# Kernel tuning notes

Hardware: AMD Instinct MI355X
Metric: run time of the kernel (lower is better)

The kernel has to match this reference:

```python
import jax, jax.numpy as jnp
import numpy as np

N_NODES = 100000
N_EDGES = 1600000
IN_DIM = 128
HID = 32
HEADS = 4
OUT_DIM = 64
NEG_SLOPE = 0.2


def gat_conv(src, dst, x, W, al, ar, b, activation):
    # x: [N, F_in], W: [F_in, H*D], al/ar: [H, D], b: [H*D]
    N = x.shape[0]
    H, D = al.shape
    h = (x @ W).reshape(N, H, D)                       # [N, H, D]
    el = jnp.einsum('nhd,hd->nh', h, al)               # [N, H]
    er = jnp.einsum('nhd,hd->nh', h, ar)               # [N, H]
    e = el[src] + er[dst]                              # [E, H]
    e = jnp.where(e > 0, e, NEG_SLOPE * e)             # leaky_relu(0.2)
    # segment softmax over destination nodes
    m = jax.ops.segment_max(e, dst, num_segments=N)    # [N, H]
    m = jnp.where(jnp.isfinite(m), m, 0.0)
    ee = jnp.exp(e - m[dst])                           # [E, H]
    denom = jax.ops.segment_sum(ee, dst, num_segments=N)  # [N, H]
    alpha = ee / denom[dst]                            # [E, H]
    msg = alpha[:, :, None] * h[src]                   # [E, H, D]
    out = jax.ops.segment_sum(msg, dst, num_segments=N)   # [N, H, D]
    out = out + b.reshape(1, H, D)
    if activation is not None:
        out = activation(out)
    return out


def setup_inputs() -> dict:
    key = jax.random.key(0)
    ks = jax.random.split(key, 16)
    hw = HID * HEADS  # 128
    ow = OUT_DIM * HEADS  # 256
    s = lambda fan: 1.0 / np.sqrt(fan)
    return {
        'nfeat': jax.random.normal(ks[0], (N_NODES, IN_DIM), jnp.float32),
        'src': jax.random.randint(ks[1], (N_EDGES,), 0, N_NODES),
        'dst': jax.random.randint(ks[2], (N_EDGES,), 0, N_NODES),
        'W0': jax.random.normal(ks[3], (IN_DIM, hw), jnp.float32) * s(IN_DIM),
        'al0': jax.random.normal(ks[4], (HEADS, HID), jnp.float32) * s(HID),
        'ar0': jax.random.normal(ks[5], (HEADS, HID), jnp.float32) * s(HID),
        'b0': jnp.zeros((hw,), jnp.float32),
        'W1': jax.random.normal(ks[6], (hw, hw), jnp.float32) * s(hw),
        'al1': jax.random.normal(ks[7], (HEADS, HID), jnp.float32) * s(HID),
        'ar1': jax.random.normal(ks[8], (HEADS, HID), jnp.float32) * s(HID),
        'b1': jnp.zeros((hw,), jnp.float32),
        'W2': jax.random.normal(ks[9], (hw, ow), jnp.float32) * s(hw),
        'al2': jax.random.normal(ks[10], (HEADS, OUT_DIM), jnp.float32) * s(OUT_DIM),
        'ar2': jax.random.normal(ks[11], (HEADS, OUT_DIM), jnp.float32) * s(OUT_DIM),
        'b2': jnp.zeros((ow,), jnp.float32),
    }


def reference(nfeat, src, dst, W0, al0, ar0, b0, W1, al1, ar1, b1, W2, al2, ar2, b2):
    h = nfeat
    # hidden layers: elu activation, flatten heads
    h = gat_conv(src, dst, h, W0, al0, ar0, b0, jax.nn.elu).reshape(N_NODES, -1)
    h = gat_conv(src, dst, h, W1, al1, ar1, b1, jax.nn.elu).reshape(N_NODES, -1)
    # output layer: no activation, mean over heads
    out = gat_conv(src, dst, h, W2, al2, ar2, b2, None).mean(axis=1)  # [N, OUT_DIM]
    return out
```

## Files before the change

kernel.cpp:

```cpp
#include <hip/hip_runtime.h>
#include <hip/hip_bf16.h>
#include <cstddef>
#include <cstdint>

#define N_NODES 100000
#define N_EDGES 1600000
#define NPASS 4

typedef __attribute__((ext_vector_type(8))) short bf16x8;
typedef __attribute__((ext_vector_type(4))) float f32x4;
typedef __attribute__((ext_vector_type(2))) _Float16 half2_t;
typedef __attribute__((ext_vector_type(4))) _Float16 half4_t;

__device__ inline unsigned short f2bf(float x) {
    unsigned int u = __float_as_uint(x);
    unsigned int r = (u + 0x7fffu + ((u >> 16) & 1u)) >> 16;
    return (unsigned short)r;
}
__device__ inline float bf2f(unsigned short b) {
    return __uint_as_float((unsigned int)b << 16);
}
__device__ inline unsigned short f2h_bits(float x) {
    _Float16 h = (_Float16)x;
    return __builtin_bit_cast(unsigned short, h);
}

__global__ void hist_kernel(const int* __restrict__ dst, int* __restrict__ deg) {
    int e = blockIdx.x * 256 + threadIdx.x;
    if (e < N_EDGES) atomicAdd(&deg[dst[e]], 1);
}

__global__ void scan_block_kernel(const int* __restrict__ deg, int* __restrict__ rowptr,
                                  int* __restrict__ bsum) {
    __shared__ int s[256];
    int t = threadIdx.x;
    int base = blockIdx.x * 1024 + t * 4;
    int v[4]; int sum = 0;
#pragma unroll
    for (int j = 0; j < 4; ++j) { v[j] = (base + j < N_NODES) ? deg[base + j] : 0; sum += v[j]; }
    s[t] = sum; __syncthreads();
    for (int off = 1; off < 256; off <<= 1) {
        int x = (t >= off) ? s[t - off] : 0;
        __syncthreads();
        s[t] += x;
        __syncthreads();
    }
    int excl = (t > 0) ? s[t - 1] : 0;
    if (t == 255) bsum[blockIdx.x] = s[255];
    int run = excl;
#pragma unroll
    for (int j = 0; j < 4; ++j) { if (base + j < N_NODES) rowptr[base + j] = run; run += v[j]; }
}

__global__ void scan_bsum_kernel(int* bsum, int nb) {
    __shared__ int s[128];
    int t = threadIdx.x;
    int v = (t < nb) ? bsum[t] : 0;
    s[t] = v; __syncthreads();
    for (int off = 1; off < 128; off <<= 1) {
        int x = (t >= off) ? s[t - off] : 0;
        __syncthreads();
        s[t] += x;
        __syncthreads();
    }
    if (t < nb) bsum[t] = (t > 0) ? s[t - 1] : 0;
}

__global__ void scan_add_kernel(int* __restrict__ rowptr, const int* __restrict__ bsum) {
    int i = blockIdx.x * 256 + threadIdx.x;
    if (i < N_NODES) rowptr[i] += bsum[i >> 10];
    if (i == 0) rowptr[N_NODES] = N_EDGES;
}

__global__ __launch_bounds__(256) void scatter_pass_kernel(
    const int* __restrict__ src, const int* __restrict__ dst,
    const int* __restrict__ rowptr, int* __restrict__ fill,
    int* __restrict__ csr_src, int lo, int hi) {
    int e = blockIdx.x * 256 + threadIdx.x;
    if (e >= N_EDGES) return;
    int d = dst[e];
    if (d >= lo && d < hi) {
        int pos = rowptr[d] + atomicAdd(&fill[d], 1);
        csr_src[pos] = src[e];
    }
}

__global__ __launch_bounds__(256) void convert_w_kernel(const float* __restrict__ W,
                                                        unsigned short* __restrict__ Wth,
                                                        unsigned short* __restrict__ Wtl,
                                                        int Ncols) {
    int t = blockIdx.x * 256 + threadIdx.x;
    if (t >= 128 * Ncols) return;
    int n = t >> 7, k = t & 127;
    float x = W[(size_t)k * Ncols + n];
    unsigned short h = f2bf(x);
    unsigned short l = f2bf(x - bf2f(h));
    Wth[t] = h;
    Wtl[t] = l;
}

template <int DHEAD, bool FP32IN>
__global__ __launch_bounds__(256) void mfma_gemm_kernel(
    const unsigned short* __restrict__ Xhi, const unsigned short* __restrict__ Xlo,
    const float* __restrict__ Xf,
    const unsigned short* __restrict__ Wth, const unsigned short* __restrict__ Wtl,
    float* __restrict__ el, float* __restrict__ er, _Float16* __restrict__ Hh,
    int M, int ldH, const float* __restrict__ alv, const float* __restrict__ arv) {
    __shared__ unsigned short AH[128 * 136];
    __shared__ unsigned short AL[128 * 136];
    const int tid = threadIdx.x;
    const int wave = tid >> 6, lane = tid & 63;
    const int r = lane & 15, kg = lane >> 4;
    const int row0 = blockIdx.x * 128;
    const int col0 = blockIdx.y * 128;

    if constexpr (FP32IN) {
#pragma unroll
        for (int i = 0; i < 16; ++i) {
            int idx = i * 256 + tid;
            int rr = idx >> 5;
            int u = idx & 31;
            int grow = row0 + rr;
            if (grow > M - 1) grow = M - 1;
            float4 v = *reinterpret_cast<const float4*>(Xf + (size_t)grow * 128 + u * 4);
            unsigned short h0 = f2bf(v.x), h1 = f2bf(v.y), h2 = f2bf(v.z), h3 = f2bf(v.w);
            unsigned short l0 = f2bf(v.x - bf2f(h0)), l1 = f2bf(v.y - bf2f(h1));
            unsigned short l2 = f2bf(v.z - bf2f(h2)), l3 = f2bf(v.w - bf2f(h3));
            unsigned int* hp = reinterpret_cast<unsigned int*>(&AH[rr * 136 + u * 4]);
            hp[0] = (unsigned int)h0 | ((unsigned int)h1 << 16);
            hp[1] = (unsigned int)h2 | ((unsigned int)h3 << 16);
            unsigned int* lp = reinterpret_cast<unsigned int*>(&AL[rr * 136 + u * 4]);
            lp[0] = (unsigned int)l0 | ((unsigned int)l1 << 16);
            lp[1] = (unsigned int)l2 | ((unsigned int)l3 << 16);
        }
    } else {
#pragma unroll
        for (int i = 0; i < 16; ++i) {
            int sa = i * 256 + tid;
            int a = sa >> 11;
            int s = sa & 2047;
            int rr = s >> 4;
            int u = s & 15;
            const unsigned short* srcp = (a ? Xlo : Xhi) + (size_t)(row0 + rr) * 128 + u * 8;
            unsigned short* dstp = (a ? AL : AH) + rr * 136 + u * 8;
            *reinterpret_cast<uint4*>(dstp) = *reinterpret_cast<const uint4*>(srcp);
        }
    }
    __syncthreads();

    f32x4 acc[2][8];
#pragma unroll
    for (int rt = 0; rt < 2; ++rt)
#pragma unroll
        for (int ct = 0; ct < 8; ++ct)
            acc[rt][ct] = (f32x4){0.f, 0.f, 0.f, 0.f};

#pragma unroll
    for (int ks = 0; ks < 4; ++ks) {
        bf16x8 bh[8], bl[8];
#pragma unroll
        for (int ct = 0; ct < 8; ++ct) {
            size_t off = (size_t)(col0 + ct * 16 + r) * 128 + ks * 32 + kg * 8;
            bh[ct] = *reinterpret_cast<const bf16x8*>(Wth + off);
            bl[ct] = *reinterpret_cast<const bf16x8*>(Wtl + off);
        }
#pragma unroll
        for (int rt = 0; rt < 2; ++rt) {
            int lrow = wave * 32 + rt * 16 + r;
            bf16x8 ah = *reinterpret_cast<const bf16x8*>(&AH[lrow * 136 + ks * 32 + kg * 8]);
            bf16x8 al8 = *reinterpret_cast<const bf16x8*>(&AL[lrow * 136 + ks * 32 + kg * 8]);
#pragma unroll
            for (int ct = 0; ct < 8; ++ct) {
                acc[rt][ct] = __builtin_amdgcn_mfma_f32_16x16x32_bf16(ah, bh[ct], acc[rt][ct], 0, 0, 0);
                acc[rt][ct] = __builtin_amdgcn_mfma_f32_16x16x32_bf16(al8, bh[ct], acc[rt][ct], 0, 0, 0);
                acc[rt][ct] = __builtin_amdgcn_mfma_f32_16x16x32_bf16(ah, bl[ct], acc[rt][ct], 0, 0, 0);
            }
        }
    }

    constexpr int CTH = DHEAD / 16;
    constexpr int HB = 8 / CTH;
    float als[8], ars[8];
#pragma unroll
    for (int ct = 0; ct < 8; ++ct) {
        als[ct] = alv[col0 + ct * 16 + r];
        ars[ct] = arv[col0 + ct * 16 + r];
    }
    f32x4 pel[2][HB], per_[2][HB];
#pragma unroll
    for (int rt = 0; rt < 2; ++rt)
#pragma unroll
        for (int hl = 0; hl < HB; ++hl) {
            pel[rt][hl] = (f32x4){0.f, 0.f, 0.f, 0.f};
            per_[rt][hl] = (f32x4){0.f, 0.f, 0.f, 0.f};
        }
#pragma unroll
    for (int rt = 0; rt < 2; ++rt)
#pragma unroll
        for (int ct = 0; ct < 8; ++ct) {
            pel[rt][ct / CTH] += acc[rt][ct] * als[ct];
            per_[rt][ct / CTH] += acc[rt][ct] * ars[ct];
        }
#pragma unroll
    for (int off = 1; off < 16; off <<= 1) {
#pragma unroll
        for (int rt = 0; rt < 2; ++rt)
#pragma unroll
            for (int hl = 0; hl < HB; ++hl)
#pragma unroll
                for (int j = 0; j < 4; ++j) {
                    pel[rt][hl][j] += __shfl_xor(pel[rt][hl][j], off);
                    per_[rt][hl][j] += __shfl_xor(per_[rt][hl][j], off);
                }
    }
#pragma unroll
    for (int hl = 0; hl < HB; ++hl) {
        if (r == hl) {
            int hg = col0 / DHEAD + hl;
#pragma unroll
            for (int rt = 0; rt < 2; ++rt)
#pragma unroll
                for (int j = 0; j < 4; ++j) {
                    int grow = row0 + wave * 32 + rt * 16 + kg * 4 + j;
                    if (grow < M) {
                        el[(size_t)grow * 4 + hg] = pel[rt][hl][j];
                        er[(size_t)grow * 4 + hg] = per_[rt][hl][j];
                    }
                }
        }
    }

    __syncthreads();
#pragma unroll
    for (int rt = 0; rt < 2; ++rt)
#pragma unroll
        for (int ct = 0; ct < 8; ++ct)
#pragma unroll
            for (int j = 0; j < 4; ++j) {
                int lrow = wave * 32 + rt * 16 + kg * 4 + j;
                AH[lrow * 136 + ct * 16 + r] = f2h_bits(acc[rt][ct][j]);
            }
    __syncthreads();
#pragma unroll
    for (int it = 0; it < 8; ++it) {
        int idx = it * 256 + tid;
        int rr = idx >> 4;
        int c8 = idx & 15;
        int grow = row0 + rr;
        if (grow < M)
            *reinterpret_cast<uint4*>(Hh + (size_t)grow * ldH + col0 + c8 * 8) =
                *reinterpret_cast<const uint4*>(&AH[rr * 136 + c8 * 8]);
    }
}

template <int F, int MODE>
__global__ __launch_bounds__(256) void sgather_kernel(
    const _Float16* __restrict__ hfeat, const float* __restrict__ el,
    const float* __restrict__ er, const int* __restrict__ rowptr,
    const int* __restrict__ csr_src, const float* __restrict__ bias,
    float* __restrict__ out, unsigned short* __restrict__ ohi,
    unsigned short* __restrict__ olo) {
    constexpr int V = F / 64;
    constexpr int D = F / 4;
    __shared__ float wsh[4][256];
    int wv = threadIdx.x >> 6;
    int wid = (blockIdx.x * 256 + threadIdx.x) >> 6;
    int lane = threadIdx.x & 63;
    if (wid >= N_NODES) return;
    int row0 = rowptr[wid], row1 = rowptr[wid + 1];
    int f0 = lane * V;
    int hh = lane >> 4;
    float4 ern = *reinterpret_cast<const float4*>(er + (size_t)wid * 4);

    float ac0[V], ac1[V], ac2[V], ac3[V];
#pragma unroll
    for (int v = 0; v < V; ++v) { ac0[v] = 0.f; ac1[v] = 0.f; ac2[v] = 0.f; ac3[v] = 0.f; }
    float den = 0.f;

    for (int base = row0; base < row1; base += 64) {
        int i = base + lane;
        int sv = (i < row1) ? csr_src[i] : 0;
        float4 e4 = *reinterpret_cast<const float4*>(el + (size_t)sv * 4);
        float4 es;
        es.x = e4.x + ern.x; es.x = es.x > 0.f ? es.x : 0.2f * es.x; es.x = __expf(es.x);
        es.y = e4.y + ern.y; es.y = es.y > 0.f ? es.y : 0.2f * es.y; es.y = __expf(es.y);
        es.z = e4.z + ern.z; es.z = es.z > 0.f ? es.z : 0.2f * es.z; es.z = __expf(es.z);
        es.w = e4.w + ern.w; es.w = es.w > 0.f ? es.w : 0.2f * es.w; es.w = __expf(es.w);
        *reinterpret_cast<float4*>(&wsh[wv][lane * 4]) = es;

        int cnt = min(64, row1 - base);
        const float* wp = &wsh[wv][hh];
        int j = 0;
        for (; j + 4 <= cnt; j += 4) {
            int s0 = __shfl(sv, j), s1 = __shfl(sv, j + 1);
            int s2 = __shfl(sv, j + 2), s3 = __shfl(sv, j + 3);
            float w0 = wp[(j + 0) * 4], w1 = wp[(j + 1) * 4];
            float w2 = wp[(j + 2) * 4], w3 = wp[(j + 3) * 4];
            den += (w0 + w1) + (w2 + w3);
            if (V == 4) {
                half4_t a = *reinterpret_cast<const half4_t*>(hfeat + (size_t)s0 * F + f0);
                half4_t b = *reinterpret_cast<const half4_t*>(hfeat + (size_t)s1 * F + f0);
                half4_t c = *reinterpret_cast<const half4_t*>(hfeat + (size_t)s2 * F + f0);
                half4_t d = *reinterpret_cast<const half4_t*>(hfeat + (size_t)s3 * F + f0);
#pragma unroll
                for (int v = 0; v < V; ++v) {
                    ac0[v] = fmaf(w0, (float)a[v], ac0[v]);
                    ac1[v] = fmaf(w1, (float)b[v], ac1[v]);
                    ac2[v] = fmaf(w2, (float)c[v], ac2[v]);
                    ac3[v] = fmaf(w3, (float)d[v], ac3[v]);
                }
            } else {
                half2_t a = *reinterpret_cast<const half2_t*>(hfeat + (size_t)s0 * F + f0);
                half2_t b = *reinterpret_cast<const half2_t*>(hfeat + (size_t)s1 * F + f0);
                half2_t c = *reinterpret_cast<const half2_t*>(hfeat + (size_t)s2 * F + f0);
                half2_t d = *reinterpret_cast<const half2_t*>(hfeat + (size_t)s3 * F + f0);
#pragma unroll
                for (int v = 0; v < V; ++v) {
                    ac0[v] = fmaf(w0, (float)a[v], ac0[v]);
                    ac1[v] = fmaf(w1, (float)b[v], ac1[v]);
                    ac2[v] = fmaf(w2, (float)c[v], ac2[v]);
                    ac3[v] = fmaf(w3, (float)d[v], ac3[v]);
                }
            }
        }
        for (; j < cnt; ++j) {
            int s0 = __shfl(sv, j);
            float w0 = wp[(size_t)j * 4];
            den += w0;
            if (V == 4) {
                half4_t a = *reinterpret_cast<const half4_t*>(hfeat + (size_t)s0 * F + f0);
#pragma unroll
                for (int v = 0; v < V; ++v) ac0[v] = fmaf(w0, (float)a[v], ac0[v]);
            } else {
                half2_t a = *reinterpret_cast<const half2_t*>(hfeat + (size_t)s0 * F + f0);
#pragma unroll
                for (int v = 0; v < V; ++v) ac0[v] = fmaf(w0, (float)a[v], ac0[v]);
            }
        }
    }

    float inv = den > 0.f ? 1.f / den : 0.f;
    float val[V];
#pragma unroll
    for (int v = 0; v < V; ++v)
        val[v] = ((ac0[v] + ac1[v]) + (ac2[v] + ac3[v])) * inv + bias[f0 + v];

    if (MODE == 0) {
#pragma unroll
        for (int v = 0; v < V; ++v)
            val[v] = val[v] > 0.f ? val[v] : (__expf(val[v]) - 1.f);
        unsigned short h0 = f2bf(val[0]), h1 = f2bf(val[1]);
        unsigned short l0 = f2bf(val[0] - bf2f(h0)), l1 = f2bf(val[1] - bf2f(h1));
        reinterpret_cast<unsigned int*>(ohi)[(size_t)wid * (F / 2) + lane] =
            (unsigned int)h0 | ((unsigned int)h1 << 16);
        reinterpret_cast<unsigned int*>(olo)[(size_t)wid * (F / 2) + lane] =
            (unsigned int)l0 | ((unsigned int)l1 << 16);
    } else {
#pragma unroll
        for (int v = 0; v < V; ++v) {
            val[v] += __shfl_xor(val[v], 16);
            val[v] += __shfl_xor(val[v], 32);
        }
        if (lane < 16) {
            float4 o = make_float4(val[0] * 0.25f, val[1] * 0.25f, val[2] * 0.25f, val[3] * 0.25f);
            *reinterpret_cast<float4*>(out + (size_t)wid * D + lane * 4) = o;
        }
    }
}

extern "C" void kernel_launch(void* const* d_in, const int* in_sizes, int n_in,
                              void* d_out, int out_size, void* d_ws, size_t ws_size,
                              hipStream_t stream) {
    const float* nfeat = (const float*)d_in[0];
    const int* src = (const int*)d_in[1];
    const int* dst = (const int*)d_in[2];
    const float* W0 = (const float*)d_in[3];
    const float* al0 = (const float*)d_in[4];
    const float* ar0 = (const float*)d_in[5];
    const float* b0 = (const float*)d_in[6];
    const float* W1 = (const float*)d_in[7];
    const float* al1 = (const float*)d_in[8];
    const float* ar1 = (const float*)d_in[9];
    const float* b1 = (const float*)d_in[10];
    const float* W2 = (const float*)d_in[11];
    const float* al2 = (const float*)d_in[12];
    const float* ar2 = (const float*)d_in[13];
    const float* b2 = (const float*)d_in[14];
    float* out = (float*)d_out;

    char* w = (char*)d_ws;
    unsigned short* XA_hi = (unsigned short*)w; w += (size_t)N_NODES * 128 * 2;
    unsigned short* XA_lo = (unsigned short*)w; w += (size_t)N_NODES * 128 * 2;
    unsigned short* XB_hi = (unsigned short*)w; w += (size_t)N_NODES * 128 * 2;
    unsigned short* XB_lo = (unsigned short*)w; w += (size_t)N_NODES * 128 * 2;
    _Float16* Ph01 = (_Float16*)w; w += (size_t)N_NODES * 128 * 2;
    float* el = (float*)w;     w += (size_t)N_NODES * 4 * 4;
    float* er = (float*)w;     w += (size_t)N_NODES * 4 * 4;
    int* rowptr = (int*)w;     w += (size_t)(N_NODES + 4) * 4;
    int* deg = (int*)w;        w += (size_t)N_NODES * 4;
    int* bsum = (int*)w;       w += 256 * 4;
    int* csr_src = (int*)w;    w += (size_t)N_EDGES * 4;
    unsigned short* Wt0h = (unsigned short*)w; w += 16384 * 2;
    unsigned short* Wt0l = (unsigned short*)w; w += 16384 * 2;
    unsigned short* Wt1h = (unsigned short*)w; w += 16384 * 2;
    unsigned short* Wt1l = (unsigned short*)w; w += 16384 * 2;
    unsigned short* Wt2h = (unsigned short*)w; w += 32768 * 2;
    unsigned short* Wt2l = (unsigned short*)w; w += 32768 * 2;

    _Float16* H2h = (_Float16*)XB_hi;

    const int nb_scan = (N_NODES + 1023) / 1024;

    convert_w_kernel<<<64, 256, 0, stream>>>(W0, Wt0h, Wt0l, 128);
    convert_w_kernel<<<64, 256, 0, stream>>>(W1, Wt1h, Wt1l, 128);
    convert_w_kernel<<<128, 256, 0, stream>>>(W2, Wt2h, Wt2l, 256);

    hipMemsetAsync(deg, 0, (size_t)N_NODES * 4, stream);
    hist_kernel<<<(N_EDGES + 255) / 256, 256, 0, stream>>>(dst, deg);
    scan_block_kernel<<<nb_scan, 256, 0, stream>>>(deg, rowptr, bsum);
    scan_bsum_kernel<<<1, 128, 0, stream>>>(bsum, nb_scan);
    scan_add_kernel<<<(N_NODES + 256) / 256, 256, 0, stream>>>(rowptr, bsum);
    hipMemsetAsync(deg, 0, (size_t)N_NODES * 4, stream);
    {
        const int eb = (N_EDGES + 255) / 256;
        const int rs = (N_NODES + NPASS - 1) / NPASS;
        for (int p = 0; p < NPASS; ++p)
            scatter_pass_kernel<<<eb, 256, 0, stream>>>(src, dst, rowptr, deg, csr_src,
                                                        p * rs, min((p + 1) * rs, N_NODES));
    }

    const int nw_blocks = (N_NODES + 3) / 4;
    dim3 gg1(782, 1), gg2(782, 2);

    mfma_gemm_kernel<32, true><<<gg1, 256, 0, stream>>>(nullptr, nullptr, nfeat, Wt0h, Wt0l,
                                                        el, er, Ph01, N_NODES, 128, al0, ar0);
    sgather_kernel<128, 0><<<nw_blocks, 256, 0, stream>>>(Ph01, el, er, rowptr, csr_src, b0,
                                                          nullptr, XB_hi, XB_lo);

    mfma_gemm_kernel<32, false><<<gg1, 256, 0, stream>>>(XB_hi, XB_lo, nullptr, Wt1h, Wt1l,
                                                         el, er, Ph01, N_NODES, 128, al1, ar1);
    sgather_kernel<128, 0><<<nw_blocks, 256, 0, stream>>>(Ph01, el, er, rowptr, csr_src, b1,
                                                          nullptr, XA_hi, XA_lo);

    mfma_gemm_kernel<64, false><<<gg2, 256, 0, stream>>>(XA_hi, XA_lo, nullptr, Wt2h, Wt2l,
                                                         el, er, H2h, N_NODES, 256, al2, ar2);
    sgather_kernel<256, 1><<<nw_blocks, 256, 0, stream>>>(H2h, el, er, rowptr, csr_src, b2,
                                                          out, nullptr, nullptr);
}
```

Measured before the change: 673.7 us.

## Map one node per half-wave in gather kernels with wider feature loads

The softmax-aggregation gather kernel now assigns each destination node to 32 lanes instead of a full 64-lane wave. Edge chunks and shuffles are sized to 32, and each lane loads and accumulates twice as many features with 8- or 4-wide half-precision vector loads. With an average degree near 16, this is meant to stop most lanes sitting idle during per-edge weight computation and to halve the number of waves. The cost is possible divergence when the two nodes sharing a wave have different degrees, plus more registers per lane.

```diff
diff --git a/kernel.cpp b/kernel.cpp
--- a/kernel.cpp
+++ b/kernel.cpp
@@ -11,6 +11,7 @@
 typedef __attribute__((ext_vector_type(4))) float f32x4;
 typedef __attribute__((ext_vector_type(2))) _Float16 half2_t;
 typedef __attribute__((ext_vector_type(4))) _Float16 half4_t;
+typedef __attribute__((ext_vector_type(8))) _Float16 half8_t;
 
 __device__ inline unsigned short f2bf(float x) {
     unsigned int u = __float_as_uint(x);
@@ -254,22 +255,24 @@
 }
 
 template <int F, int MODE>
-__global__ __launch_bounds__(256) void sgather_kernel(
+__global__ __launch_bounds__(256) void sgather2_kernel(
     const _Float16* __restrict__ hfeat, const float* __restrict__ el,
     const float* __restrict__ er, const int* __restrict__ rowptr,
     const int* __restrict__ csr_src, const float* __restrict__ bias,
     float* __restrict__ out, unsigned short* __restrict__ ohi,
     unsigned short* __restrict__ olo) {
-    constexpr int V = F / 64;
+    constexpr int V = F / 32;
     constexpr int D = F / 4;
-    __shared__ float wsh[4][256];
+    __shared__ float wsh[4][2][128];
     int wv = threadIdx.x >> 6;
-    int wid = (blockIdx.x * 256 + threadIdx.x) >> 6;
     int lane = threadIdx.x & 63;
+    int hw = lane >> 5;
+    int hl = lane & 31;
+    int wid = blockIdx.x * 8 + (threadIdx.x >> 5);
     if (wid >= N_NODES) return;
     int row0 = rowptr[wid], row1 = rowptr[wid + 1];
-    int f0 = lane * V;
-    int hh = lane >> 4;
+    int f0 = hl * V;
+    int hh = hl >> 3;
     float4 ern = *reinterpret_cast<const float4*>(er + (size_t)wid * 4);
 
     float ac0[V], ac1[V], ac2[V], ac3[V];
@@ -277,8 +280,8 @@
     for (int v = 0; v < V; ++v) { ac0[v] = 0.f; ac1[v] = 0.f; ac2[v] = 0.f; ac3[v] = 0.f; }
     float den = 0.f;
 
-    for (int base = row0; base < row1; base += 64) {
-        int i = base + lane;
+    for (int base = row0; base < row1; base += 32) {
+        int i = base + hl;
         int sv = (i < row1) ? csr_src[i] : 0;
         float4 e4 = *reinterpret_cast<const float4*>(el + (size_t)sv * 4);
         float4 es;
@@ -286,22 +289,24 @@
         es.y = e4.y + ern.y; es.y = es.y > 0.f ? es.y : 0.2f * es.y; es.y = __expf(es.y);
         es.z = e4.z + ern.z; es.z = es.z > 0.f ? es.z : 0.2f * es.z; es.z = __expf(es.z);
         es.w = e4.w + ern.w; es.w = es.w > 0.f ? es.w : 0.2f * es.w; es.w = __expf(es.w);
-        *reinterpret_cast<float4*>(&wsh[wv][lane * 4]) = es;
-
-        int cnt = min(64, row1 - base);
-        const float* wp = &wsh[wv][hh];
+        asm volatile("" ::: "memory");
+        *reinterpret_cast<float4*>(&wsh[wv][hw][hl * 4]) = es;
+        asm volatile("" ::: "memory");
+
+        int cnt = min(32, row1 - base);
+        const float* wp = &wsh[wv][hw][hh];
         int j = 0;
         for (; j + 4 <= cnt; j += 4) {
-            int s0 = __shfl(sv, j), s1 = __shfl(sv, j + 1);
-            int s2 = __shfl(sv, j + 2), s3 = __shfl(sv, j + 3);
+            int s0 = __shfl(sv, j, 32), s1 = __shfl(sv, j + 1, 32);
+            int s2 = __shfl(sv, j + 2, 32), s3 = __shfl(sv, j + 3, 32);
             float w0 = wp[(j + 0) * 4], w1 = wp[(j + 1) * 4];
             float w2 = wp[(j + 2) * 4], w3 = wp[(j + 3) * 4];
             den += (w0 + w1) + (w2 + w3);
-            if (V == 4) {
-                half4_t a = *reinterpret_cast<const half4_t*>(hfeat + (size_t)s0 * F + f0);
-                half4_t b = *reinterpret_cast<const half4_t*>(hfeat + (size_t)s1 * F + f0);
-                half4_t c = *reinterpret_cast<const half4_t*>(hfeat + (size_t)s2 * F + f0);
-                half4_t d = *reinterpret_cast<const half4_t*>(hfeat + (size_t)s3 * F + f0);
+            if (V == 8) {
+                half8_t a = *reinterpret_cast<const half8_t*>(hfeat + (size_t)s0 * F + f0);
+                half8_t b = *reinterpret_cast<const half8_t*>(hfeat + (size_t)s1 * F + f0);
+                half8_t c = *reinterpret_cast<const half8_t*>(hfeat + (size_t)s2 * F + f0);
+                half8_t d = *reinterpret_cast<const half8_t*>(hfeat + (size_t)s3 * F + f0);
 #pragma unroll
                 for (int v = 0; v < V; ++v) {
                     ac0[v] = fmaf(w0, (float)a[v], ac0[v]);
@@ -310,10 +315,10 @@
                     ac3[v] = fmaf(w3, (float)d[v], ac3[v]);
                 }
             } else {
-                half2_t a = *reinterpret_cast<const half2_t*>(hfeat + (size_t)s0 * F + f0);
-                half2_t b = *reinterpret_cast<const half2_t*>(hfeat + (size_t)s1 * F + f0);
-                half2_t c = *reinterpret_cast<const half2_t*>(hfeat + (size_t)s2 * F + f0);
-                half2_t d = *reinterpret_cast<const half2_t*>(hfeat + (size_t)s3 * F + f0);
+                half4_t a = *reinterpret_cast<const half4_t*>(hfeat + (size_t)s0 * F + f0);
+                half4_t b = *reinterpret_cast<const half4_t*>(hfeat + (size_t)s1 * F + f0);
+                half4_t c = *reinterpret_cast<const half4_t*>(hfeat + (size_t)s2 * F + f0);
+                half4_t d = *reinterpret_cast<const half4_t*>(hfeat + (size_t)s3 * F + f0);
 #pragma unroll
                 for (int v = 0; v < V; ++v) {
                     ac0[v] = fmaf(w0, (float)a[v], ac0[v]);
@@ -324,19 +329,20 @@
             }
         }
         for (; j < cnt; ++j) {
-            int s0 = __shfl(sv, j);
+            int s0 = __shfl(sv, j, 32);
             float w0 = wp[(size_t)j * 4];
             den += w0;
-            if (V == 4) {
-                half4_t a = *reinterpret_cast<const half4_t*>(hfeat + (size_t)s0 * F + f0);
+            if (V == 8) {
+                half8_t a = *reinterpret_cast<const half8_t*>(hfeat + (size_t)s0 * F + f0);
 #pragma unroll
                 for (int v = 0; v < V; ++v) ac0[v] = fmaf(w0, (float)a[v], ac0[v]);
             } else {
-                half2_t a = *reinterpret_cast<const half2_t*>(hfeat + (size_t)s0 * F + f0);
+                half4_t a = *reinterpret_cast<const half4_t*>(hfeat + (size_t)s0 * F + f0);
 #pragma unroll
                 for (int v = 0; v < V; ++v) ac0[v] = fmaf(w0, (float)a[v], ac0[v]);
             }
         }
+        asm volatile("" ::: "memory");
     }
 
     float inv = den > 0.f ? 1.f / den : 0.f;
@@ -349,21 +355,28 @@
 #pragma unroll
         for (int v = 0; v < V; ++v)
             val[v] = val[v] > 0.f ? val[v] : (__expf(val[v]) - 1.f);
-        unsigned short h0 = f2bf(val[0]), h1 = f2bf(val[1]);
-        unsigned short l0 = f2bf(val[0] - bf2f(h0)), l1 = f2bf(val[1] - bf2f(h1));
-        reinterpret_cast<unsigned int*>(ohi)[(size_t)wid * (F / 2) + lane] =
-            (unsigned int)h0 | ((unsigned int)h1 << 16);
-        reinterpret_cast<unsigned int*>(olo)[(size_t)wid * (F / 2) + lane] =
-            (unsigned int)l0 | ((unsigned int)l1 << 16);
+        unsigned int hpk[2], lpk[2];
+#pragma unroll
+        for (int q = 0; q < 2; ++q) {
+            unsigned short h0 = f2bf(val[2 * q]), h1 = f2bf(val[2 * q + 1]);
+            unsigned short l0 = f2bf(val[2 * q] - bf2f(h0));
+            unsigned short l1 = f2bf(val[2 * q + 1] - bf2f(h1));
+            hpk[q] = (unsigned int)h0 | ((unsigned int)h1 << 16);
+            lpk[q] = (unsigned int)l0 | ((unsigned int)l1 << 16);
+        }
+        *reinterpret_cast<uint2*>(ohi + (size_t)wid * F + f0) = make_uint2(hpk[0], hpk[1]);
+        *reinterpret_cast<uint2*>(olo + (size_t)wid * F + f0) = make_uint2(lpk[0], lpk[1]);
     } else {
 #pragma unroll
         for (int v = 0; v < V; ++v) {
+            val[v] += __shfl_xor(val[v], 8);
             val[v] += __shfl_xor(val[v], 16);
-            val[v] += __shfl_xor(val[v], 32);
-        }
-        if (lane < 16) {
-            float4 o = make_float4(val[0] * 0.25f, val[1] * 0.25f, val[2] * 0.25f, val[3] * 0.25f);
-            *reinterpret_cast<float4*>(out + (size_t)wid * D + lane * 4) = o;
+        }
+        if (hl < 8) {
+            float4 o0 = make_float4(val[0] * 0.25f, val[1] * 0.25f, val[2] * 0.25f, val[3] * 0.25f);
+            float4 o1 = make_float4(val[4] * 0.25f, val[5] * 0.25f, val[6] * 0.25f, val[7] * 0.25f);
+            *reinterpret_cast<float4*>(out + (size_t)wid * D + hl * 8) = o0;
+            *reinterpret_cast<float4*>(out + (size_t)wid * D + hl * 8 + 4) = o1;
         }
     }
 }
@@ -429,21 +442,21 @@
                                                         p * rs, min((p + 1) * rs, N_NODES));
     }
 
-    const int nw_blocks = (N_NODES + 3) / 4;
+    const int ng_blocks = (N_NODES + 7) / 8;
     dim3 gg1(782, 1), gg2(782, 2);
 
     mfma_gemm_kernel<32, true><<<gg1, 256, 0, stream>>>(nullptr, nullptr, nfeat, Wt0h, Wt0l,
                                                         el, er, Ph01, N_NODES, 128, al0, ar0);
-    sgather_kernel<128, 0><<<nw_blocks, 256, 0, stream>>>(Ph01, el, er, rowptr, csr_src, b0,
-                                                          nullptr, XB_hi, XB_lo);
+    sgather2_kernel<128, 0><<<ng_blocks, 256, 0, stream>>>(Ph01, el, er, rowptr, csr_src, b0,
+                                                           nullptr, XB_hi, XB_lo);
 
     mfma_gemm_kernel<32, false><<<gg1, 256, 0, stream>>>(XB_hi, XB_lo, nullptr, Wt1h, Wt1l,
                                                          el, er, Ph01, N_NODES, 128, al1, ar1);
-    sgather_kernel<128, 0><<<nw_blocks, 256, 0, stream>>>(Ph01, el, er, rowptr, csr_src, b1,
-                                                          nullptr, XA_hi, XA_lo);
+    sgather2_kernel<128, 0><<<ng_blocks, 256, 0, stream>>>(Ph01, el, er, rowptr, csr_src, b1,
+                                                           nullptr, XA_hi, XA_lo);
 
     mfma_gemm_kernel<64, false><<<gg2, 256, 0, stream>>>(XA_hi, XA_lo, nullptr, Wt2h, Wt2l,
                                                          el, er, H2h, N_NODES, 256, al2, ar2);
-    sgather_kernel<256, 1><<<nw_blocks, 256, 0, stream>>>(H2h, el, er, rowptr, csr_src, b2,
-                                                          out, nullptr, nullptr);
-}
+    sgather2_kernel<256, 1><<<ng_blocks, 256, 0, stream>>>(H2h, el, er, rowptr, csr_src, b2,
+                                                           out, nullptr, nullptr);
+}
```

New measurement: 665.9 us. No clear change (-1.2%).
